# Kernel optimization log

Measured on AMD Instinct MI355X. Metric: run time of the kernel, lower is better.

Reference implementation:

```python
import jax, jax.numpy as jnp
import numpy as np

NEG_INF = -10000000000.0
TEMPERATURE = 0.5
N_NODES = 100000
N_EDGES = 3200000
DIM = 32


def setup_inputs() -> dict:
    key = jax.random.key(0)
    ks = jax.random.split(key, 8)
    node_reps = jax.random.normal(ks[0], (N_NODES, DIM), dtype=jnp.float32)
    edge_reps = jax.random.normal(ks[1], (N_EDGES, DIM), dtype=jnp.float32)
    graph_rep = jax.random.normal(ks[2], (DIM,), dtype=jnp.float32)
    subgraph_rep = jax.random.normal(ks[3], (DIM,), dtype=jnp.float32)
    W1 = jax.random.normal(ks[4], (3 * DIM, DIM), dtype=jnp.float32) / np.sqrt(3 * DIM)
    b1 = jax.random.normal(ks[5], (DIM,), dtype=jnp.float32) * 0.01
    edge_index = jax.random.randint(ks[6], (2, N_EDGES), 0, N_NODES, dtype=jnp.int64)
    selection = jax.random.randint(ks[7], (N_EDGES,), 0, 2) > 0
    return {"node_reps": node_reps, "edge_reps": edge_reps, "graph_rep": graph_rep,
            "subgraph_rep": subgraph_rep, "W1": W1, "b1": b1,
            "edge_index": edge_index, "selection": selection}


def reference(node_reps, edge_reps, graph_rep, subgraph_rep, W1, b1, edge_index, selection):
    # gather per-edge endpoint reps: [E, 32] each
    src = node_reps[edge_index[0]]
    dst = node_reps[edge_index[1]]
    tmp = jnp.concatenate([src, dst, edge_reps], axis=1)  # [E, 96]
    edge_action_reps = jax.nn.elu(tmp @ W1 + b1)          # Linear(96,32)+ELU
    graph_diff_rep = graph_rep - subgraph_rep             # [32]
    score = edge_action_reps @ graph_diff_rep             # [E]
    score = jnp.where(selection, NEG_INF, score)          # mask already-selected edges
    return jax.nn.softmax(score / TEMPERATURE)
```

## Files before the change

kernel.cpp:

```cpp
#include <hip/hip_runtime.h>

#define E_EDGES 3200000
#define N_NODES_K 100000
#define NEG_INF_F (-10000000000.0f)
#define KE_NB (E_EDGES / 256)

typedef __attribute__((ext_vector_type(8))) short short8v;
typedef __attribute__((ext_vector_type(4))) float floatx4;

__device__ __forceinline__ unsigned packbf2(float a, float b) {
    unsigned ua = __float_as_uint(a), ub = __float_as_uint(b);
    ua = (ua + 0x7fffu + ((ua >> 16) & 1u)) >> 16;
    ub = (ub + 0x7fffu + ((ub >> 16) & 1u)) & 0xffff0000u;
    return ub | ua;
}

__global__ __launch_bounds__(256) void k_nodeproj(
    const float* __restrict__ nr, const float* __restrict__ W1,
    const float* __restrict__ b1, unsigned* __restrict__ P1c,
    unsigned* __restrict__ P2c, const unsigned* __restrict__ ei_w,
    const unsigned* __restrict__ sel_w, int* __restrict__ flags) {
    if (blockIdx.x == 0 && threadIdx.x < 64) {
        const int lane = threadIdx.x;
        unsigned hw = ei_w[2 * (lane + 1) + 1];
        unsigned long long anyhi = __ballot(hw != 0u);
        unsigned sv = sel_w[lane];
        unsigned long long not01 = __ballot(sv != 0u && sv != 1u);
        unsigned long long notf  = __ballot(sv != 0u && sv != 0x3F800000u);
        if (lane == 0) {
            flags[0] = (anyhi == 0ull) ? 1 : 0;
            flags[1] = (not01 == 0ull) ? 0 : ((notf == 0ull) ? 2 : 1);
        }
    }
    int n = blockIdx.x * 256 + threadIdx.x;
    if (n >= N_NODES_K) return;
    const float4* x4 = (const float4*)(nr + (size_t)n * 32);
    float xr[32];
#pragma unroll
    for (int i = 0; i < 8; ++i) {
        float4 t = x4[i];
        xr[4 * i + 0] = t.x; xr[4 * i + 1] = t.y; xr[4 * i + 2] = t.z; xr[4 * i + 3] = t.w;
    }
    float a1[32], a2[32];
#pragma unroll
    for (int j = 0; j < 32; ++j) { a1[j] = b1[j]; a2[j] = 0.0f; }
#pragma unroll
    for (int k = 0; k < 32; ++k) {
        const float xv = xr[k];
#pragma unroll
        for (int jb = 0; jb < 8; ++jb) {
            const float4 w1 = *(const float4*)(W1 + (size_t)k * 32 + jb * 4);
            const float4 w2 = *(const float4*)(W1 + (size_t)(32 + k) * 32 + jb * 4);
            a1[4 * jb + 0] = fmaf(xv, w1.x, a1[4 * jb + 0]);
            a1[4 * jb + 1] = fmaf(xv, w1.y, a1[4 * jb + 1]);
            a1[4 * jb + 2] = fmaf(xv, w1.z, a1[4 * jb + 2]);
            a1[4 * jb + 3] = fmaf(xv, w1.w, a1[4 * jb + 3]);
            a2[4 * jb + 0] = fmaf(xv, w2.x, a2[4 * jb + 0]);
            a2[4 * jb + 1] = fmaf(xv, w2.y, a2[4 * jb + 1]);
            a2[4 * jb + 2] = fmaf(xv, w2.z, a2[4 * jb + 2]);
            a2[4 * jb + 3] = fmaf(xv, w2.w, a2[4 * jb + 3]);
        }
    }
    unsigned r1[16], r2[16];
#pragma unroll
    for (int j = 0; j < 16; ++j) {
        r1[j] = packbf2(a1[j], a1[j + 16]);
        r2[j] = packbf2(a2[j], a2[j + 16]);
    }
    uint4* o1 = (uint4*)(P1c + (size_t)n * 16);
    uint4* o2 = (uint4*)(P2c + (size_t)n * 16);
#pragma unroll
    for (int i = 0; i < 4; ++i) {
        o1[i] = ((const uint4*)r1)[i];
        o2[i] = ((const uint4*)r2)[i];
    }
}

__global__ __launch_bounds__(256) void k_edge(
    const float* __restrict__ er_, const float* __restrict__ W1,
    const float* __restrict__ gr, const float* __restrict__ sgr,
    const void* __restrict__ ei_raw, const void* __restrict__ sel_raw,
    const int* __restrict__ flags,
    const unsigned* __restrict__ P1c, const unsigned* __restrict__ P2c,
    float* __restrict__ scores, float* __restrict__ bmax,
    float* __restrict__ bsum) {
    __shared__ int sIdx[256];
    __shared__ int dIdx[256];
    __shared__ int aAct[256];
    __shared__ float sred[8];

    const int tid = threadIdx.x;
    const int e0 = blockIdx.x * 256;
    const int fei = flags[0], fsel = flags[1];

    bool act;
    if (fsel == 0)
        act = __builtin_nontemporal_load((const int*)sel_raw + e0 + tid) == 0;
    else if (fsel == 1)
        act = __builtin_nontemporal_load((const unsigned char*)sel_raw + e0 + tid) == 0;
    else
        act = __builtin_nontemporal_load((const float*)sel_raw + e0 + tid) == 0.0f;

    int s = 0, d = 0;
    if (act) {
        if (fei) {
            s = __builtin_nontemporal_load((const int*)ei_raw + 2 * (size_t)(e0 + tid));
            d = __builtin_nontemporal_load((const int*)ei_raw +
                                           2 * ((size_t)E_EDGES + e0 + tid));
        } else {
            s = __builtin_nontemporal_load((const int*)ei_raw + e0 + tid);
            d = __builtin_nontemporal_load((const int*)ei_raw + E_EDGES + e0 + tid);
        }
    }
    sIdx[tid] = s; dIdx[tid] = d; aAct[tid] = act ? 1 : 0;

    const int lane = tid & 63;
    const int wv   = tid >> 6;
    const int col  = lane & 15;
    const int g    = lane >> 4;
    const int kb   = g * 8;

    union { unsigned u[4]; short8v v; } A0, A1;
#pragma unroll
    for (int t = 0; t < 4; ++t) {
        float x0 = W1[(size_t)(64 + kb + 2 * t) * 32 + col];
        float x1 = W1[(size_t)(64 + kb + 2 * t + 1) * 32 + col];
        A0.u[t] = packbf2(x0, x1);
        float y0 = W1[(size_t)(64 + kb + 2 * t) * 32 + 16 + col];
        float y1 = W1[(size_t)(64 + kb + 2 * t + 1) * 32 + 16 + col];
        A1.u[t] = packbf2(y0, y1);
    }
    float gd0[4], gd1[4];
#pragma unroll
    for (int r = 0; r < 4; ++r) {
        gd0[r] = gr[g * 4 + r] - sgr[g * 4 + r];
        gd1[r] = gr[16 + g * 4 + r] - sgr[16 + g * 4 + r];
    }
    __syncthreads();

    float s_loc[4];
#pragma unroll
    for (int t = 0; t < 4; ++t) {
        const int erow = (wv * 4 + t) * 16 + col;
        const bool ea = aAct[erow] != 0;

        union { unsigned u[4]; short8v v; } B;
        B.u[0] = 0u; B.u[1] = 0u; B.u[2] = 0u; B.u[3] = 0u;
        if (ea) {
            const floatx4* ep = (const floatx4*)(er_ + (size_t)(e0 + erow) * 32 + kb);
            floatx4 xa = __builtin_nontemporal_load(ep);
            floatx4 xb = __builtin_nontemporal_load(ep + 1);
            B.u[0] = packbf2(xa.x, xa.y); B.u[1] = packbf2(xa.z, xa.w);
            B.u[2] = packbf2(xb.x, xb.y); B.u[3] = packbf2(xb.z, xb.w);
        }

        floatx4 acc0 = {0.f, 0.f, 0.f, 0.f}, acc1 = {0.f, 0.f, 0.f, 0.f};
        acc0 = __builtin_amdgcn_mfma_f32_16x16x32_bf16(A0.v, B.v, acc0, 0, 0, 0);
        acc1 = __builtin_amdgcn_mfma_f32_16x16x32_bf16(A1.v, B.v, acc1, 0, 0, 0);

        uint4 u1 = make_uint4(0u, 0u, 0u, 0u), u2 = make_uint4(0u, 0u, 0u, 0u);
        if (ea) {
            u1 = *(const uint4*)(P1c + (size_t)sIdx[erow] * 16 + g * 4);
            u2 = *(const uint4*)(P2c + (size_t)dIdx[erow] * 16 + g * 4);
        }
        const unsigned* pu1 = (const unsigned*)&u1;
        const unsigned* pu2 = (const unsigned*)&u2;
        float part = 0.0f;
#pragma unroll
        for (int r = 0; r < 4; ++r) {
            float z0 = acc0[r] + __uint_as_float(pu1[r] << 16)
                               + __uint_as_float(pu2[r] << 16);
            float z1 = acc1[r] + __uint_as_float(pu1[r] & 0xffff0000u)
                               + __uint_as_float(pu2[r] & 0xffff0000u);
            float h0 = z0 > 0.0f ? z0 : (__expf(z0) - 1.0f);
            float h1 = z1 > 0.0f ? z1 : (__expf(z1) - 1.0f);
            part = fmaf(h0, gd0[r], part);
            part = fmaf(h1, gd1[r], part);
        }
        part += __shfl_xor(part, 16);
        part += __shfl_xor(part, 32);
        float sc = ea ? part : NEG_INF_F;
        s_loc[t] = sc;
        if (g == 0) scores[e0 + erow] = sc;
    }

    float m = fmaxf(fmaxf(s_loc[0], s_loc[1]), fmaxf(s_loc[2], s_loc[3]));
#pragma unroll
    for (int off = 32; off > 0; off >>= 1) m = fmaxf(m, __shfl_down(m, off));
    if (lane == 0) sred[wv] = m;
    __syncthreads();
    const float mb = fmaxf(fmaxf(sred[0], sred[1]), fmaxf(sred[2], sred[3]));
    float v = 0.0f;
    if (g == 0) {
#pragma unroll
        for (int t = 0; t < 4; ++t) v += __expf((s_loc[t] - mb) * 2.0f);
    }
#pragma unroll
    for (int off = 32; off > 0; off >>= 1) v += __shfl_down(v, off);
    __syncthreads();
    if (lane == 0) sred[4 + wv] = v;
    __syncthreads();
    if (tid == 0) {
        bmax[blockIdx.x] = mb;
        bsum[blockIdx.x] = sred[4] + sred[5] + sred[6] + sred[7];
    }
}

__global__ __launch_bounds__(256) void k_reduce(
    const float* __restrict__ bmax, const float* __restrict__ bsum,
    float* __restrict__ mx_out, float* __restrict__ rsum_out) {
    const int tid = threadIdx.x;
    __shared__ float sm[4];
    float m = -3.0e38f;
    for (int i = tid; i < KE_NB; i += 256) m = fmaxf(m, bmax[i]);
#pragma unroll
    for (int off = 32; off > 0; off >>= 1) m = fmaxf(m, __shfl_down(m, off));
    const int lane = tid & 63, wid = tid >> 6;
    if (lane == 0) sm[wid] = m;
    __syncthreads();
    const float M = fmaxf(fmaxf(sm[0], sm[1]), fmaxf(sm[2], sm[3]));
    float s = 0.0f;
    for (int i = tid; i < KE_NB; i += 256)
        s += bsum[i] * __expf((bmax[i] - M) * 2.0f);
#pragma unroll
    for (int off = 32; off > 0; off >>= 1) s += __shfl_down(s, off);
    __syncthreads();
    __shared__ float ss[4];
    if (lane == 0) ss[wid] = s;
    __syncthreads();
    if (tid == 0) {
        *mx_out = M;
        *rsum_out = 1.0f / (ss[0] + ss[1] + ss[2] + ss[3]);
    }
}

__global__ __launch_bounds__(256) void k_fin(
    const float* __restrict__ scores, const float* __restrict__ mx,
    const float* __restrict__ rsum, float* __restrict__ out) {
    const int i = blockIdx.x * 256 + threadIdx.x;
    const float M = *mx;
    const float r = *rsum;
    float4 s = ((const float4*)scores)[i];
    float4 o;
    o.x = __expf((s.x - M) * 2.0f) * r;
    o.y = __expf((s.y - M) * 2.0f) * r;
    o.z = __expf((s.z - M) * 2.0f) * r;
    o.w = __expf((s.w - M) * 2.0f) * r;
    ((float4*)out)[i] = o;
}

extern "C" void kernel_launch(void* const* d_in, const int* in_sizes, int n_in,
                              void* d_out, int out_size, void* d_ws, size_t ws_size,
                              hipStream_t stream) {
    const float* node_reps    = (const float*)d_in[0];
    const float* edge_reps    = (const float*)d_in[1];
    const float* graph_rep    = (const float*)d_in[2];
    const float* subgraph_rep = (const float*)d_in[3];
    const float* W1           = (const float*)d_in[4];
    const float* b1           = (const float*)d_in[5];
    const void*  ei           = d_in[6];
    const void*  selp         = d_in[7];
    float* out = (float*)d_out;

    char* ws = (char*)d_ws;
    size_t off = 0;
    unsigned* P1c = (unsigned*)(ws + off); off += (size_t)N_NODES_K * 64;
    unsigned* P2c = (unsigned*)(ws + off); off += (size_t)N_NODES_K * 64;
    float* scores = (float*)(ws + off);    off += (size_t)E_EDGES * 4;
    float* bmax   = (float*)(ws + off);    off += (size_t)KE_NB * 4;
    float* bsum   = (float*)(ws + off);    off += (size_t)KE_NB * 4;
    int*   flags  = (int*)(ws + off);      off += 64;
    float* mx     = (float*)(ws + off);    off += 4;
    float* rsum   = (float*)(ws + off);    off += 4;

    k_nodeproj<<<(N_NODES_K + 255) / 256, 256, 0, stream>>>(
        node_reps, W1, b1, P1c, P2c,
        (const unsigned*)ei, (const unsigned*)selp, flags);
    k_edge<<<KE_NB, 256, 0, stream>>>(edge_reps, W1, graph_rep, subgraph_rep,
                                      ei, selp, flags, P1c, P2c, scores, bmax, bsum);
    k_reduce<<<1, 256, 0, stream>>>(bmax, bsum, mx, rsum);
    k_fin<<<E_EDGES / 4 / 256, 256, 0, stream>>>(scores, mx, rsum, out);
}
```

Measured before the change: 139.3 us.

## Use MFMA for node projection, hoist gathers, widen reduce, nontemporal score stores

The node projection kernel now runs on bf16 MFMA, with each wave handling 16 nodes, instead of 64 scalar FMAs per output per thread. In the edge kernel the P1c/P2c gathers are issued alongside the edge-rep loads, before the MFMAs, so their latency overlaps the matrix work. Score stores become nontemporal, and the single-block reduction uses 1024 threads instead of 256. The node projection now rounds its inputs and weights to bf16 before multiplying rather than only at the output, which slightly changes precision.

```diff
diff --git a/kernel.cpp b/kernel.cpp
--- a/kernel.cpp
+++ b/kernel.cpp
@@ -4,6 +4,7 @@
 #define N_NODES_K 100000
 #define NEG_INF_F (-10000000000.0f)
 #define KE_NB (E_EDGES / 256)
+#define NP_NB ((N_NODES_K + 63) / 64)
 
 typedef __attribute__((ext_vector_type(8))) short short8v;
 typedef __attribute__((ext_vector_type(4))) float floatx4;
@@ -32,47 +33,48 @@
             flags[1] = (not01 == 0ull) ? 0 : ((notf == 0ull) ? 2 : 1);
         }
     }
-    int n = blockIdx.x * 256 + threadIdx.x;
-    if (n >= N_NODES_K) return;
-    const float4* x4 = (const float4*)(nr + (size_t)n * 32);
-    float xr[32];
-#pragma unroll
-    for (int i = 0; i < 8; ++i) {
-        float4 t = x4[i];
-        xr[4 * i + 0] = t.x; xr[4 * i + 1] = t.y; xr[4 * i + 2] = t.z; xr[4 * i + 3] = t.w;
-    }
-    float a1[32], a2[32];
-#pragma unroll
-    for (int j = 0; j < 32; ++j) { a1[j] = b1[j]; a2[j] = 0.0f; }
-#pragma unroll
-    for (int k = 0; k < 32; ++k) {
-        const float xv = xr[k];
-#pragma unroll
-        for (int jb = 0; jb < 8; ++jb) {
-            const float4 w1 = *(const float4*)(W1 + (size_t)k * 32 + jb * 4);
-            const float4 w2 = *(const float4*)(W1 + (size_t)(32 + k) * 32 + jb * 4);
-            a1[4 * jb + 0] = fmaf(xv, w1.x, a1[4 * jb + 0]);
-            a1[4 * jb + 1] = fmaf(xv, w1.y, a1[4 * jb + 1]);
-            a1[4 * jb + 2] = fmaf(xv, w1.z, a1[4 * jb + 2]);
-            a1[4 * jb + 3] = fmaf(xv, w1.w, a1[4 * jb + 3]);
-            a2[4 * jb + 0] = fmaf(xv, w2.x, a2[4 * jb + 0]);
-            a2[4 * jb + 1] = fmaf(xv, w2.y, a2[4 * jb + 1]);
-            a2[4 * jb + 2] = fmaf(xv, w2.z, a2[4 * jb + 2]);
-            a2[4 * jb + 3] = fmaf(xv, w2.w, a2[4 * jb + 3]);
-        }
-    }
-    unsigned r1[16], r2[16];
-#pragma unroll
-    for (int j = 0; j < 16; ++j) {
-        r1[j] = packbf2(a1[j], a1[j + 16]);
-        r2[j] = packbf2(a2[j], a2[j + 16]);
-    }
-    uint4* o1 = (uint4*)(P1c + (size_t)n * 16);
-    uint4* o2 = (uint4*)(P2c + (size_t)n * 16);
-#pragma unroll
-    for (int i = 0; i < 4; ++i) {
-        o1[i] = ((const uint4*)r1)[i];
-        o2[i] = ((const uint4*)r2)[i];
+    const int tid  = threadIdx.x;
+    const int lane = tid & 63;
+    const int wv   = tid >> 6;
+    const int col  = lane & 15;
+    const int g    = lane >> 4;
+    const int kb   = g * 8;
+    const int n0   = blockIdx.x * 64 + wv * 16;
+
+    int nrow = n0 + col;
+    if (nrow >= N_NODES_K) nrow = N_NODES_K - 1;
+    const float4* ap = (const float4*)(nr + (size_t)nrow * 32 + kb);
+    float4 av0 = ap[0], av1 = ap[1];
+    union { unsigned u[4]; short8v v; } A;
+    A.u[0] = packbf2(av0.x, av0.y); A.u[1] = packbf2(av0.z, av0.w);
+    A.u[2] = packbf2(av1.x, av1.y); A.u[3] = packbf2(av1.z, av1.w);
+
+    union { unsigned u[4]; short8v v; } B1lo, B1hi, B2lo, B2hi;
+#pragma unroll
+    for (int t = 0; t < 4; ++t) {
+        const size_t r0 = (size_t)(kb + 2 * t) * 32, r1 = r0 + 32;
+        B1lo.u[t] = packbf2(W1[r0 + col],          W1[r1 + col]);
+        B1hi.u[t] = packbf2(W1[r0 + 16 + col],     W1[r1 + 16 + col]);
+        const size_t s0 = (size_t)(32 + kb + 2 * t) * 32, s1 = s0 + 32;
+        B2lo.u[t] = packbf2(W1[s0 + col],          W1[s1 + col]);
+        B2hi.u[t] = packbf2(W1[s0 + 16 + col],     W1[s1 + 16 + col]);
+    }
+    const float blo = b1[col], bhi = b1[16 + col];
+
+    floatx4 a1lo = {0.f,0.f,0.f,0.f}, a1hi = {0.f,0.f,0.f,0.f};
+    floatx4 a2lo = {0.f,0.f,0.f,0.f}, a2hi = {0.f,0.f,0.f,0.f};
+    a1lo = __builtin_amdgcn_mfma_f32_16x16x32_bf16(A.v, B1lo.v, a1lo, 0, 0, 0);
+    a1hi = __builtin_amdgcn_mfma_f32_16x16x32_bf16(A.v, B1hi.v, a1hi, 0, 0, 0);
+    a2lo = __builtin_amdgcn_mfma_f32_16x16x32_bf16(A.v, B2lo.v, a2lo, 0, 0, 0);
+    a2hi = __builtin_amdgcn_mfma_f32_16x16x32_bf16(A.v, B2hi.v, a2hi, 0, 0, 0);
+
+#pragma unroll
+    for (int r = 0; r < 4; ++r) {
+        const int n = n0 + g * 4 + r;
+        if (n < N_NODES_K) {
+            P1c[(size_t)n * 16 + col] = packbf2(a1lo[r] + blo, a1hi[r] + bhi);
+            P2c[(size_t)n * 16 + col] = packbf2(a2lo[r], a2hi[r]);
+        }
     }
 }
 
@@ -146,10 +148,13 @@
 
         union { unsigned u[4]; short8v v; } B;
         B.u[0] = 0u; B.u[1] = 0u; B.u[2] = 0u; B.u[3] = 0u;
+        uint4 u1 = make_uint4(0u, 0u, 0u, 0u), u2 = make_uint4(0u, 0u, 0u, 0u);
         if (ea) {
             const floatx4* ep = (const floatx4*)(er_ + (size_t)(e0 + erow) * 32 + kb);
             floatx4 xa = __builtin_nontemporal_load(ep);
             floatx4 xb = __builtin_nontemporal_load(ep + 1);
+            u1 = *(const uint4*)(P1c + (size_t)sIdx[erow] * 16 + g * 4);
+            u2 = *(const uint4*)(P2c + (size_t)dIdx[erow] * 16 + g * 4);
             B.u[0] = packbf2(xa.x, xa.y); B.u[1] = packbf2(xa.z, xa.w);
             B.u[2] = packbf2(xb.x, xb.y); B.u[3] = packbf2(xb.z, xb.w);
         }
@@ -158,11 +163,6 @@
         acc0 = __builtin_amdgcn_mfma_f32_16x16x32_bf16(A0.v, B.v, acc0, 0, 0, 0);
         acc1 = __builtin_amdgcn_mfma_f32_16x16x32_bf16(A1.v, B.v, acc1, 0, 0, 0);
 
-        uint4 u1 = make_uint4(0u, 0u, 0u, 0u), u2 = make_uint4(0u, 0u, 0u, 0u);
-        if (ea) {
-            u1 = *(const uint4*)(P1c + (size_t)sIdx[erow] * 16 + g * 4);
-            u2 = *(const uint4*)(P2c + (size_t)dIdx[erow] * 16 + g * 4);
-        }
         const unsigned* pu1 = (const unsigned*)&u1;
         const unsigned* pu2 = (const unsigned*)&u2;
         float part = 0.0f;
@@ -181,7 +181,7 @@
         part += __shfl_xor(part, 32);
         float sc = ea ? part : NEG_INF_F;
         s_loc[t] = sc;
-        if (g == 0) scores[e0 + erow] = sc;
+        if (g == 0) __builtin_nontemporal_store(sc, scores + e0 + erow);
     }
 
     float m = fmaxf(fmaxf(s_loc[0], s_loc[1]), fmaxf(s_loc[2], s_loc[3]));
@@ -206,31 +206,35 @@
     }
 }
 
-__global__ __launch_bounds__(256) void k_reduce(
+__global__ __launch_bounds__(1024) void k_reduce(
     const float* __restrict__ bmax, const float* __restrict__ bsum,
     float* __restrict__ mx_out, float* __restrict__ rsum_out) {
     const int tid = threadIdx.x;
-    __shared__ float sm[4];
     float m = -3.0e38f;
-    for (int i = tid; i < KE_NB; i += 256) m = fmaxf(m, bmax[i]);
+    for (int i = tid; i < KE_NB; i += 1024) m = fmaxf(m, bmax[i]);
 #pragma unroll
     for (int off = 32; off > 0; off >>= 1) m = fmaxf(m, __shfl_down(m, off));
+    __shared__ float sm[16];
+    __shared__ float ss[16];
     const int lane = tid & 63, wid = tid >> 6;
     if (lane == 0) sm[wid] = m;
     __syncthreads();
-    const float M = fmaxf(fmaxf(sm[0], sm[1]), fmaxf(sm[2], sm[3]));
-    float s = 0.0f;
-    for (int i = tid; i < KE_NB; i += 256)
-        s += bsum[i] * __expf((bmax[i] - M) * 2.0f);
-#pragma unroll
-    for (int off = 32; off > 0; off >>= 1) s += __shfl_down(s, off);
-    __syncthreads();
-    __shared__ float ss[4];
-    if (lane == 0) ss[wid] = s;
+    float M = -3.0e38f;
+#pragma unroll
+    for (int i = 0; i < 16; ++i) M = fmaxf(M, sm[i]);
+    float sum = 0.0f;
+    for (int i = tid; i < KE_NB; i += 1024)
+        sum += bsum[i] * __expf((bmax[i] - M) * 2.0f);
+#pragma unroll
+    for (int off = 32; off > 0; off >>= 1) sum += __shfl_down(sum, off);
+    if (lane == 0) ss[wid] = sum;
     __syncthreads();
     if (tid == 0) {
+        float tot = 0.0f;
+#pragma unroll
+        for (int i = 0; i < 16; ++i) tot += ss[i];
         *mx_out = M;
-        *rsum_out = 1.0f / (ss[0] + ss[1] + ss[2] + ss[3]);
+        *rsum_out = 1.0f / tot;
     }
 }
 
@@ -273,11 +277,11 @@
     float* mx     = (float*)(ws + off);    off += 4;
     float* rsum   = (float*)(ws + off);    off += 4;
 
-    k_nodeproj<<<(N_NODES_K + 255) / 256, 256, 0, stream>>>(
+    k_nodeproj<<<NP_NB, 256, 0, stream>>>(
         node_reps, W1, b1, P1c, P2c,
         (const unsigned*)ei, (const unsigned*)selp, flags);
     k_edge<<<KE_NB, 256, 0, stream>>>(edge_reps, W1, graph_rep, subgraph_rep,
                                       ei, selp, flags, P1c, P2c, scores, bmax, bsum);
-    k_reduce<<<1, 256, 0, stream>>>(bmax, bsum, mx, rsum);
+    k_reduce<<<1, 1024, 0, stream>>>(bmax, bsum, mx, rsum);
     k_fin<<<E_EDGES / 4 / 256, 256, 0, stream>>>(scores, mx, rsum, out);
 }
```

Result: faster. 113.6 us (-18.4%).
